# Performance work log

Hardware: AMD Instinct MI355X
Metric: run time of the kernel (lower is better)

The kernel has to match this reference:

```python
import jax, jax.numpy as jnp
import numpy as np

VOCAB = 30
D_MODEL = 512
D_K = 64
D_V = 64
N_HEAD = 8
D_FF = 2048
N_LAYERS = 4
LN_EPS = 1e-5


def _make_pe(max_len, d_model):
    pos = np.arange(max_len, dtype=np.float32)[:, None]
    div = np.exp(np.arange(0, d_model, 2, dtype=np.float32) * (-np.log(10000.0) / d_model))
    pe = np.zeros((max_len, d_model), dtype=np.float32)
    pe[:, 0::2] = np.sin(pos * div)
    pe[:, 1::2] = np.cos(pos * div)
    return jnp.asarray(pe)


def setup_inputs() -> dict:
    key = jax.random.key(0)
    ks = jax.random.split(key, 16)
    B, S = 4, 2048
    s = 0.02
    inp = {
        "input_ids": jax.random.randint(ks[0], (B, S), 0, VOCAB, dtype=jnp.int64),
        "attn_mask": jax.random.randint(ks[1], (B, S), 0, 2, dtype=jnp.int64),
        "tok_embed": jax.random.normal(ks[2], (VOCAB, D_MODEL), jnp.float32) * s,
        "pe": _make_pe(S, D_MODEL),
        "Wq": jax.random.normal(ks[3], (N_LAYERS, D_MODEL, N_HEAD * D_K), jnp.float32) * s,
        "Wk": jax.random.normal(ks[4], (N_LAYERS, D_MODEL, N_HEAD * D_K), jnp.float32) * s,
        "Wv": jax.random.normal(ks[5], (N_LAYERS, D_MODEL, N_HEAD * D_V), jnp.float32) * s,
        "Wo": jax.random.normal(ks[6], (N_LAYERS, N_HEAD * D_V, D_MODEL), jnp.float32) * s,
        "ln1_g": jnp.ones((N_LAYERS, D_MODEL), jnp.float32),
        "ln1_b": jnp.zeros((N_LAYERS, D_MODEL), jnp.float32),
        "W1": jax.random.normal(ks[7], (N_LAYERS, D_MODEL, D_FF), jnp.float32) * s,
        "W2": jax.random.normal(ks[8], (N_LAYERS, D_FF, D_MODEL), jnp.float32) * s,
        "ln2_g": jnp.ones((N_LAYERS, D_MODEL), jnp.float32),
        "ln2_b": jnp.zeros((N_LAYERS, D_MODEL), jnp.float32),
    }
    return inp


def _layernorm(x, g, b):
    mu = jnp.mean(x, axis=-1, keepdims=True)
    var = jnp.mean(jnp.square(x - mu), axis=-1, keepdims=True)
    return (x - mu) * jax.lax.rsqrt(var + LN_EPS) * g + b


def reference(input_ids, attn_mask, tok_embed, pe, Wq, Wk, Wv, Wo, ln1_g, ln1_b, W1, W2, ln2_g, ln2_b):
    B, S = input_ids.shape
    x = tok_embed[input_ids] + pe[:S][None]  # [B,S,D]
    # pad mask: key positions where attn_mask==0, broadcast over heads & queries
    pad = (attn_mask == 0)[:, None, None, :]  # [B,1,1,S]
    scale = 1.0 / np.sqrt(D_K)
    for l in range(N_LAYERS):
        # multi-head self-attention
        q = (x @ Wq[l]).reshape(B, S, N_HEAD, D_K)
        k = (x @ Wk[l]).reshape(B, S, N_HEAD, D_K)
        v = (x @ Wv[l]).reshape(B, S, N_HEAD, D_V)
        scores = jnp.einsum('bqhd,bkhd->bhqk', q, k) * scale
        scores = jnp.where(pad, -1e9, scores)
        attn = jax.nn.softmax(scores, axis=-1)
        ctx = jnp.einsum('bhqk,bkhd->bqhd', attn, v).reshape(B, S, N_HEAD * D_V)
        x = _layernorm(ctx @ Wo[l] + x, ln1_g[l], ln1_b[l])
        # position-wise FFN
        h = jax.nn.relu(x @ W1[l])
        x = _layernorm(h @ W2[l] + x, ln2_g[l], ln2_b[l])
    return x
```

## Files before the change

### kernel.cpp

```cpp
#include <hip/hip_runtime.h>
#include <stdint.h>

#define S_LEN 2048
#define B_SZ 4
#define DM 512
#define NTOK (B_SZ * S_LEN)

typedef unsigned short u16;
typedef unsigned int u32;
typedef unsigned long long u64;
typedef __attribute__((ext_vector_type(8))) short short8;
typedef __attribute__((ext_vector_type(4))) float f32x4;

typedef const __attribute__((address_space(1))) u32 gq_t;
typedef __attribute__((address_space(3))) u32 lq_t;

__device__ __forceinline__ u16 f2bf(float f) {
  union { float f; u32 u; } v; v.f = f;
  return (u16)((v.u + 0x7FFFu + ((v.u >> 16) & 1u)) >> 16);
}

__device__ __forceinline__ float bf2f(u32 hi16_at_lo) {
  union { u32 u; float f; } v; v.u = hi16_at_lo;
  return v.f;
}

__device__ __forceinline__ float fexp2(float x) {
#if __has_builtin(__builtin_amdgcn_exp2f)
  return __builtin_amdgcn_exp2f(x);
#else
  return exp2f(x);
#endif
}

__device__ __forceinline__ short8 mk8(u64 a, u64 b) {
  union { u64 q[2]; short8 s; } u;
  u.q[0] = a; u.q[1] = b;
  return u.s;
}

__device__ __forceinline__ void swap32(u32& x, u32& y) {
  asm("v_permlane32_swap_b32 %0, %1" : "+v"(x), "+v"(y));
}
__device__ __forceinline__ void swap16(u32& x, u32& y, int lane) {
#if __has_builtin(__builtin_amdgcn_permlane16_swap)
  asm("v_permlane16_swap_b32 %0, %1" : "+v"(x), "+v"(y));
#else
  u32 tx = __builtin_amdgcn_ds_swizzle(x, 0x401F);
  u32 ty = __builtin_amdgcn_ds_swizzle(y, 0x401F);
  bool up = (lane & 16) != 0;
  u32 nx = up ? ty : x;
  u32 ny = up ? y : tx;
  x = nx; y = ny;
#endif
}

__global__ void embed_kernel(const int* __restrict__ ids, const float* __restrict__ te,
                             const float* __restrict__ pe, u16* __restrict__ xb) {
  int gid = blockIdx.x * 256 + threadIdx.x;
  int tok = gid >> 7, c4 = (gid & 127) << 2;
  int s = tok & (S_LEN - 1);
  int id = ids[tok];
  const float4 a = *(const float4*)(te + (long)id * DM + c4);
  const float4 p = *(const float4*)(pe + (long)s * DM + c4);
  uint2 pk;
  pk.x = (u32)f2bf(a.x + p.x) | ((u32)f2bf(a.y + p.y) << 16);
  pk.y = (u32)f2bf(a.z + p.z) | ((u32)f2bf(a.w + p.w) << 16);
  *(uint2*)(xb + (long)tok * DM + c4) = pk;
}

__global__ void wconv_all(const float* __restrict__ Wq, const float* __restrict__ Wk,
                          const float* __restrict__ Wv, const float* __restrict__ Wo,
                          const float* __restrict__ W1, const float* __restrict__ W2,
                          u16* __restrict__ WqkvT, u16* __restrict__ WoT,
                          u16* __restrict__ W1T, u16* __restrict__ W2T) {
  __shared__ u16 t_lds[64 * 65];
  const int tile = blockIdx.x;
  const float* src; u16* dst; int N, K, kt, nt, l;
  if (tile < 768) {
    int which = tile >> 8, r = tile & 255;
    l = r >> 6; int rr = r & 63; kt = rr >> 3; nt = rr & 7;
    src = (which == 0 ? Wq : which == 1 ? Wk : Wv) + (long)l * 512 * 512;
    N = 512; K = 512;
    dst = WqkvT + (long)l * 1536 * 512 + (long)(which * 512) * 512;
  } else if (tile < 1024) {
    int r = tile - 768;
    l = r >> 6; int rr = r & 63; kt = rr >> 3; nt = rr & 7;
    src = Wo + (long)l * 512 * 512; N = 512; K = 512;
    dst = WoT + (long)l * 512 * 512;
  } else if (tile < 2048) {
    int r = tile - 1024;
    l = r >> 8; int rr = r & 255; kt = rr >> 5; nt = rr & 31;
    src = W1 + (long)l * 512 * 2048; N = 2048; K = 512;
    dst = W1T + (long)l * 2048 * 512;
  } else {
    int r = tile - 2048;
    l = r >> 8; int rr = r & 255; kt = rr >> 3; nt = rr & 7;
    src = W2 + (long)l * 2048 * 512; N = 512; K = 2048;
    dst = W2T + (long)l * 512 * 2048;
  }
  const int tr = threadIdx.x >> 4;
  const int tc = (threadIdx.x & 15) << 2;
#pragma unroll
  for (int i = 0; i < 4; ++i) {
    int k = tr + i * 16;
    const float4 v = *(const float4*)(src + (long)(kt * 64 + k) * N + nt * 64 + tc);
    t_lds[(tc + 0) * 65 + k] = f2bf(v.x);
    t_lds[(tc + 1) * 65 + k] = f2bf(v.y);
    t_lds[(tc + 2) * 65 + k] = f2bf(v.z);
    t_lds[(tc + 3) * 65 + k] = f2bf(v.w);
  }
  __syncthreads();
#pragma unroll
  for (int i = 0; i < 4; ++i) {
    int n = tr + i * 16;
    u16 a0 = t_lds[n * 65 + tc + 0];
    u16 a1 = t_lds[n * 65 + tc + 1];
    u16 a2 = t_lds[n * 65 + tc + 2];
    u16 a3 = t_lds[n * 65 + tc + 3];
    uint2 pk;
    pk.x = (u32)a0 | ((u32)a1 << 16);
    pk.y = (u32)a2 | ((u32)a3 << 16);
    *(uint2*)(dst + (long)(nt * 64 + n) * K + kt * 64 + tc) = pk;
  }
}

template <int BM, int BN, bool RELU, bool VSPLIT, bool SWAPC>
__global__ __launch_bounds__(BM * 2) void gemm_kernel(const u16* __restrict__ A,
                                                      const u16* __restrict__ BT,
                                                      void* __restrict__ Cout,
                                                      u16* __restrict__ vt,
                                                      int M, int N, int K) {
  constexpr int NI = BN / 32;
  constexpr int NW = BM / 32;
  constexpr int BRW = BN / NW;
  constexpr int LOADS = 4 + BRW / 8;
  __shared__ __align__(16) u16 a_t[2][BM * 64];
  __shared__ __align__(16) u16 b_t[2][BN * 64];
  const int tid = threadIdx.x;
  const int w = tid >> 6, lane = tid & 63;
  const int wr = w >> 1, wc = w & 1;
  const int g = lane >> 4, lr = lane & 15;
  const int l8 = lane >> 3, lch = lane & 7;
  const int gc = lch ^ l8;
  const int nwg = gridDim.x * gridDim.y;
  const int bid = blockIdx.x + gridDim.x * blockIdx.y;
  const int cpx = nwg >> 3;
  const int swz = (bid & 7) * cpx + (bid >> 3);
  const int bx = swz % gridDim.x, by = swz / gridDim.x;
  const long m0 = (long)by * BM, n0 = (long)bx * BN;
  f32x4 acc[4][NI] = {};
  const int nk = K >> 6;

  auto stage = [&](int nb, int kt) {
    const int k0 = kt << 6;
#pragma unroll
    for (int i = 0; i < 4; ++i) {
      int row = w * 32 + i * 8 + l8;
      __builtin_amdgcn_global_load_lds((gq_t*)(A + (m0 + row) * K + k0 + gc * 8),
                                       (lq_t*)&a_t[nb][(w * 4 + i) * 512], 16, 0, 0);
    }
#pragma unroll
    for (int i = 0; i < BRW / 8; ++i) {
      int row = w * BRW + i * 8 + l8;
      __builtin_amdgcn_global_load_lds((gq_t*)(BT + (n0 + row) * K + k0 + gc * 8),
                                       (lq_t*)&b_t[nb][(w * (BRW / 8) + i) * 512], 16, 0, 0);
    }
  };

  stage(0, 0);
  stage(1, 1);
  for (int kt = 0; kt < nk; ++kt) {
    const int cur = kt & 1;
    if (kt + 1 < nk) {
      if constexpr (LOADS == 6) asm volatile("s_waitcnt vmcnt(6)" ::: "memory");
      else                      asm volatile("s_waitcnt vmcnt(5)" ::: "memory");
    } else {
      asm volatile("s_waitcnt vmcnt(0)" ::: "memory");
    }
    __builtin_amdgcn_s_barrier();
    __builtin_amdgcn_sched_barrier(0);
    short8 af[2][4], bfr[2][NI];
#pragma unroll
    for (int ks = 0; ks < 2; ++ks) {
#pragma unroll
      for (int mi = 0; mi < 4; ++mi) {
        int row = wr * 64 + mi * 16 + lr;
        int byte = row * 128 + (((ks * 4 + g) ^ (row & 7)) << 4);
        af[ks][mi] = *(const short8*)((const char*)a_t[cur] + byte);
      }
#pragma unroll
      for (int ni = 0; ni < NI; ++ni) {
        int row = wc * (BN / 2) + ni * 16 + lr;
        int byte = row * 128 + (((ks * 4 + g) ^ (row & 7)) << 4);
        bfr[ks][ni] = *(const short8*)((const char*)b_t[cur] + byte);
      }
    }
    asm volatile("s_waitcnt lgkmcnt(0)" ::: "memory");
    __builtin_amdgcn_s_barrier();
    __builtin_amdgcn_sched_barrier(0);
    if (kt + 2 < nk) stage(cur, kt + 2);
    __builtin_amdgcn_s_setprio(1);
#pragma unroll
    for (int ks = 0; ks < 2; ++ks)
#pragma unroll
      for (int mi = 0; mi < 4; ++mi)
#pragma unroll
        for (int ni = 0; ni < NI; ++ni) {
          if constexpr (SWAPC)
            acc[mi][ni] = __builtin_amdgcn_mfma_f32_16x16x32_bf16(bfr[ks][ni], af[ks][mi], acc[mi][ni], 0, 0, 0);
          else
            acc[mi][ni] = __builtin_amdgcn_mfma_f32_16x16x32_bf16(af[ks][mi], bfr[ks][ni], acc[mi][ni], 0, 0, 0);
        }
    __builtin_amdgcn_s_setprio(0);
  }

  if constexpr (VSPLIT) {
    if (n0 >= 1024) {
#pragma unroll
      for (int mi = 0; mi < 4; ++mi)
#pragma unroll
        for (int ni = 0; ni < NI; ++ni) {
          int vc = (int)(n0 - 1024) + wc * (BN / 2) + ni * 16 + lr;
          int hh = vc >> 6, d = vc & 63;
          long tok0 = m0 + wr * 64 + mi * 16 + g * 4;
          int bb = (int)(tok0 >> 11), s0 = (int)(tok0 & 2047);
          uint2 pk;
          pk.x = (u32)f2bf(acc[mi][ni][0]) | ((u32)f2bf(acc[mi][ni][1]) << 16);
          pk.y = (u32)f2bf(acc[mi][ni][2]) | ((u32)f2bf(acc[mi][ni][3]) << 16);
          *(uint2*)(vt + (((long)bb * 8 + hh) * 64 + d) * 2048 + s0) = pk;
        }
      return;
    }
  }
  if constexpr (SWAPC) {
#pragma unroll
    for (int mi = 0; mi < 4; ++mi)
#pragma unroll
      for (int ni = 0; ni < NI; ++ni) {
        long grow = m0 + wr * 64 + mi * 16 + lr;
        long gcb = n0 + wc * (BN / 2) + ni * 16 + 4 * g;
        float v0 = acc[mi][ni][0], v1 = acc[mi][ni][1], v2 = acc[mi][ni][2], v3 = acc[mi][ni][3];
        if (RELU) {
          v0 = fmaxf(v0, 0.f); v1 = fmaxf(v1, 0.f); v2 = fmaxf(v2, 0.f); v3 = fmaxf(v3, 0.f);
        }
        uint2 pk;
        pk.x = (u32)f2bf(v0) | ((u32)f2bf(v1) << 16);
        pk.y = (u32)f2bf(v2) | ((u32)f2bf(v3) << 16);
        *(uint2*)((u16*)Cout + grow * N + gcb) = pk;
      }
  } else {
#pragma unroll
    for (int mi = 0; mi < 4; ++mi)
#pragma unroll
      for (int ni = 0; ni < NI; ++ni)
#pragma unroll
        for (int j = 0; j < 4; ++j) {
          long grow = m0 + wr * 64 + mi * 16 + g * 4 + j;
          long gcol = n0 + wc * (BN / 2) + ni * 16 + lr;
          float v = acc[mi][ni][j];
          if (RELU) v = fmaxf(v, 0.f);
          ((u16*)Cout)[grow * N + gcol] = f2bf(v);
        }
  }
}

__global__ __launch_bounds__(512) void attn_kernel(const u16* __restrict__ qkv,
                                                   const u16* __restrict__ vt,
                                                   const int* __restrict__ mask,
                                                   u16* __restrict__ ctx) {
  __shared__ __align__(16) u16 kv[2 * 4096 + 2 * 4096 + 1024];
  __shared__ __align__(16) float mvals[2][64];
  __shared__ __align__(16) float l_lds[128];
  const int tid = threadIdx.x;
  const int w = tid >> 6, lane = tid & 63;
  const int g = lane >> 4, lr = lane & 15;
  const int l8 = lane >> 3, lch = lane & 7;
  const int gc = lch ^ l8;
  const int b = blockIdx.z, h = blockIdx.y, q0 = blockIdx.x * 128;
  const long base = (long)b * S_LEN * 1536;
  const int qcol = h * 64, kcol = 512 + h * 64;
  const u16* vhead = vt + (((long)b * 8 + h) * 64) * 2048;
  u16* q_t = kv;
  u16* vone = kv + 16384;
  const float SC = 0.18033688011112042f;

  auto stageKV = [&](int nb, int kb) {
    int row = w * 8 + l8;
    __builtin_amdgcn_global_load_lds((gq_t*)(qkv + base + (long)(kb + row) * 1536 + kcol + gc * 8),
                                     (lq_t*)(kv + nb * 4096 + w * 512), 16, 0, 0);
    __builtin_amdgcn_global_load_lds((gq_t*)(vhead + (long)row * 2048 + kb + gc * 8),
                                     (lq_t*)(kv + 8192 + nb * 4096 + w * 512), 16, 0, 0);
    if (tid < 64) mvals[nb][tid] = (mask[b * S_LEN + kb + tid] == 0) ? -1e9f : 0.f;
  };

  {
    u32 val = ((tid >> 5) == 0) ? 0x3F803F80u : 0u;
    *(u32*)((char*)vone + tid * 4) = val;
  }
#pragma unroll
  for (int i = 0; i < 2; ++i) {
    int e = i * 512 + tid;
    int row = e >> 3, ch = e & 7;
    uint4 v = *(const uint4*)(qkv + base + (long)(q0 + row) * 1536 + qcol + ch * 8);
    *(uint4*)((char*)q_t + row * 128 + ((ch ^ (row & 7)) << 4)) = v;
  }
  __syncthreads();
  short8 qf[2];
#pragma unroll
  for (int ks = 0; ks < 2; ++ks) {
    int row = w * 16 + lr;
    qf[ks] = *(const short8*)((const char*)q_t + row * 128 + (((ks * 4 + g) ^ (row & 7)) << 4));
  }
  __syncthreads();
  stageKV(0, 0);
  __syncthreads();

  f32x4 o[5] = {};

  for (int kt = 0; kt < S_LEN / 64; ++kt) {
    const int cur = kt & 1;
    if (kt + 1 < S_LEN / 64) stageKV(cur ^ 1, (kt + 1) * 64);

    f32x4 s[4] = {};
    __builtin_amdgcn_s_setprio(1);
#pragma unroll
    for (int ks = 0; ks < 2; ++ks) {
#pragma unroll
      for (int ni = 0; ni < 4; ++ni) {
        int row = ni * 16 + lr;
        short8 kf = *(const short8*)((const char*)(kv + cur * 4096) + row * 128 + (((ks * 4 + g) ^ (row & 7)) << 4));
        s[ni] = __builtin_amdgcn_mfma_f32_16x16x32_bf16(kf, qf[ks], s[ni], 0, 0, 0);
      }
    }
    __builtin_amdgcn_s_setprio(0);
    float p[4][4];
#pragma unroll
    for (int ni = 0; ni < 4; ++ni) {
      const float4 mv = *(const float4*)&mvals[cur][ni * 16 + 4 * g];
      const float mva[4] = {mv.x, mv.y, mv.z, mv.w};
#pragma unroll
      for (int r = 0; r < 4; ++r)
        p[ni][r] = fexp2(fmaf(s[ni][r], SC, mva[r]));
    }
    u32 wv[4][2];
#pragma unroll
    for (int ni = 0; ni < 4; ++ni)
#pragma unroll
      for (int pp = 0; pp < 2; ++pp)
        asm("v_cvt_pk_bf16_f32 %0, %1, %2"
            : "=v"(wv[ni][pp]) : "v"(p[ni][2 * pp]), "v"(p[ni][2 * pp + 1]));

    u32 x0 = wv[0][0], x1 = wv[0][1], y0 = wv[1][0], y1 = wv[1][1];
    swap32(x0, y0); swap32(x1, y1);
    swap16(x0, y0, lane); swap16(x1, y1, lane);
    short8 pa0 = mk8((u64)x0 | ((u64)x1 << 32), (u64)y0 | ((u64)y1 << 32));
    u32 x2 = wv[2][0], x3 = wv[2][1], y2 = wv[3][0], y3 = wv[3][1];
    swap32(x2, y2); swap32(x3, y3);
    swap16(x2, y2, lane); swap16(x3, y3, lane);
    short8 pa1 = mk8((u64)x2 | ((u64)x3 << 32), (u64)y2 | ((u64)y3 << 32));

    __builtin_amdgcn_s_setprio(1);
#pragma unroll
    for (int ks2 = 0; ks2 < 2; ++ks2) {
      short8 pa = ks2 ? pa1 : pa0;
#pragma unroll
      for (int nd = 0; nd < 5; ++nd) {
        short8 vf;
        if (nd < 4) {
          int vrow = nd * 16 + lr;
          vf = *(const short8*)((const char*)(kv + 8192 + cur * 4096) + vrow * 128 + (((ks2 * 4 + g) ^ (vrow & 7)) << 4));
        } else {
          vf = *(const short8*)((const char*)vone + lr * 128 + (((ks2 * 4 + g) ^ (lr & 7)) << 4));
        }
        o[nd] = __builtin_amdgcn_mfma_f32_16x16x32_bf16(pa, vf, o[nd], 0, 0, 0);
      }
    }
    __builtin_amdgcn_s_setprio(0);
    if (kt + 1 < S_LEN / 64) __syncthreads();
  }
  if (lr == 0) {
#pragma unroll
    for (int r = 0; r < 4; ++r) l_lds[w * 16 + 4 * g + r] = o[4][r];
  }
  const float4 lv = *(const float4*)&l_lds[w * 16 + 4 * g];
  const float la[4] = {lv.x, lv.y, lv.z, lv.w};
  float inv[4];
#pragma unroll
  for (int r = 0; r < 4; ++r) inv[r] = 1.f / la[r];
#pragma unroll
  for (int nd = 0; nd < 4; ++nd)
#pragma unroll
    for (int r = 0; r < 4; ++r) {
      int tok = q0 + w * 16 + 4 * g + r;
      int col = h * 64 + nd * 16 + lr;
      ctx[((long)b * S_LEN + tok) * 512 + col] = f2bf(o[nd][r] * inv[r]);
    }
}

template <bool FINAL>
__global__ __launch_bounds__(256) void ln_kernel(const u16* __restrict__ y,
                                                 const u16* __restrict__ res,
                                                 const float* __restrict__ gam,
                                                 const float* __restrict__ bet,
                                                 u16* __restrict__ xout,
                                                 float* __restrict__ outf) {
  const int row = blockIdx.x, t = threadIdx.x;
  const long o0 = (long)row * DM;
  const u32 yb = *(const u32*)(y + o0 + 2 * t);
  const u32 rb = *(const u32*)(res + o0 + 2 * t);
  float a0 = bf2f(yb << 16) + bf2f(rb << 16);
  float a1 = bf2f(yb & 0xFFFF0000u) + bf2f(rb & 0xFFFF0000u);
  float s1 = a0 + a1, s2 = a0 * a0 + a1 * a1;
#pragma unroll
  for (int m = 32; m >= 1; m >>= 1) {
    s1 += __shfl_xor(s1, m);
    s2 += __shfl_xor(s2, m);
  }
  __shared__ float w1[4], w2[4];
  if ((t & 63) == 0) { w1[t >> 6] = s1; w2[t >> 6] = s2; }
  __syncthreads();
  s1 = w1[0] + w1[1] + w1[2] + w1[3];
  s2 = w2[0] + w2[1] + w2[2] + w2[3];
  const float mu = s1 * (1.f / DM);
  const float rstd = rsqrtf(s2 * (1.f / DM) - mu * mu + 1e-5f);
  const float2 gv = *(const float2*)&gam[2 * t];
  const float2 bv = *(const float2*)&bet[2 * t];
  float r0 = (a0 - mu) * rstd * gv.x + bv.x;
  float r1 = (a1 - mu) * rstd * gv.y + bv.y;
  if constexpr (FINAL) {
    float2 ov; ov.x = r0; ov.y = r1;
    *(float2*)&outf[o0 + 2 * t] = ov;
  } else {
    u32 pk = (u32)f2bf(r0) | ((u32)f2bf(r1) << 16);
    *(u32*)&xout[o0 + 2 * t] = pk;
  }
}

extern "C" void kernel_launch(void* const* d_in, const int* in_sizes, int n_in,
                              void* d_out, int out_size, void* d_ws, size_t ws_size,
                              hipStream_t stream) {
  const int*   ids  = (const int*)d_in[0];
  const int*   amsk = (const int*)d_in[1];
  const float* te   = (const float*)d_in[2];
  const float* pe   = (const float*)d_in[3];
  const float* Wq   = (const float*)d_in[4];
  const float* Wk   = (const float*)d_in[5];
  const float* Wv   = (const float*)d_in[6];
  const float* Wo   = (const float*)d_in[7];
  const float* ln1g = (const float*)d_in[8];
  const float* ln1b = (const float*)d_in[9];
  const float* W1   = (const float*)d_in[10];
  const float* W2   = (const float*)d_in[11];
  const float* ln2g = (const float*)d_in[12];
  const float* ln2b = (const float*)d_in[13];
  float* out = (float*)d_out;

  char* p = (char*)d_ws;
  u16* x     = (u16*)p;   p += (long)NTOK * DM * 2;
  u16* qkv   = (u16*)p;   p += (long)NTOK * 1536 * 2;
  u16* ctx   = (u16*)p;   p += (long)NTOK * DM * 2;
  u16* tmp   = (u16*)p;   p += (long)NTOK * DM * 2;
  u16* hb    = (u16*)p;   p += (long)NTOK * 2048 * 2;
  u16* WqkvT = (u16*)p;   p += (long)4 * 1536 * 512 * 2;
  u16* WoT   = (u16*)p;   p += (long)4 * 512 * 512 * 2;
  u16* W1T   = (u16*)p;   p += (long)4 * 2048 * 512 * 2;
  u16* W2T   = (u16*)p;   p += (long)4 * 512 * 2048 * 2;
  if ((size_t)(p - (char*)d_ws) > ws_size) return;
  u16* vt = hb;

  wconv_all<<<3072, 256, 0, stream>>>(Wq, Wk, Wv, Wo, W1, W2, WqkvT, WoT, W1T, W2T);
  embed_kernel<<<NTOK * 128 / 256, 256, 0, stream>>>(ids, te, pe, x);

  for (int l = 0; l < 4; ++l) {
    gemm_kernel<256, 64, false, true, false><<<dim3(1536 / 64, NTOK / 256), 512, 0, stream>>>(
        x, WqkvT + (long)l * 1536 * 512, qkv, vt, NTOK, 1536, 512);
    attn_kernel<<<dim3(S_LEN / 128, 8, B_SZ), 512, 0, stream>>>(qkv, vt, amsk, ctx);
    gemm_kernel<128, 64, false, false, true><<<dim3(512 / 64, NTOK / 128), 256, 0, stream>>>(
        ctx, WoT + (long)l * 512 * 512, tmp, nullptr, NTOK, 512, 512);
    ln_kernel<false><<<NTOK, 256, 0, stream>>>(tmp, x, ln1g + l * 512, ln1b + l * 512, x, nullptr);
    gemm_kernel<256, 64, true, false, true><<<dim3(2048 / 64, NTOK / 256), 512, 0, stream>>>(
        x, W1T + (long)l * 2048 * 512, hb, nullptr, NTOK, 2048, 512);
    gemm_kernel<128, 64, false, false, true><<<dim3(512 / 64, NTOK / 128), 256, 0, stream>>>(
        hb, W2T + (long)l * 512 * 2048, tmp, nullptr, NTOK, 512, 2048);
    if (l == 3)
      ln_kernel<true><<<NTOK, 256, 0, stream>>>(tmp, x, ln2g + l * 512, ln2b + l * 512, nullptr, out);
    else
      ln_kernel<false><<<NTOK, 256, 0, stream>>>(tmp, x, ln2g + l * 512, ln2b + l * 512, x, nullptr);
  }
}
```

Measured before the change: 593.4 us.

## Compact valid key positions so attention skips padded keys

Adds a per-batch compaction kernel that builds a list of unmasked key indices, a reverse map and a valid count. The QKV GEMM epilogue scatters V into compacted positions. The attention kernel gathers K rows through the index list and loops only over ceil(nvalid/64) key tiles, masking only the tail. Padded keys contribute exactly zero after softmax, so this drops their share of attention work. In exchange, V stores in the GEMM epilogue become scattered 2-byte writes instead of packed 8-byte writes, and an all-masked row would divide by zero.

```diff
diff --git a/kernel.cpp b/kernel.cpp
--- a/kernel.cpp
+++ b/kernel.cpp
@@ -53,6 +53,37 @@
   u32 ny = up ? y : tx;
   x = nx; y = ny;
 #endif
+}
+
+__global__ void compact_kernel(const int* __restrict__ mask, int* __restrict__ cidx,
+                               int* __restrict__ cmap, int* __restrict__ nvalid) {
+  __shared__ int wcnt[4];
+  __shared__ int running;
+  const int b = blockIdx.x, tid = threadIdx.x;
+  if (tid == 0) running = 0;
+  __syncthreads();
+  for (int c = 0; c < 8; ++c) {
+    int s = c * 256 + tid;
+    int valid = (mask[b * 2048 + s] != 0) ? 1 : 0;
+    u64 bal = __ballot(valid);
+    int lane = tid & 63, wv = tid >> 6;
+    int pre = __popcll(bal & ((1ULL << lane) - 1ULL));
+    if (lane == 0) wcnt[wv] = __popcll(bal);
+    __syncthreads();
+    int woff = running;
+    for (int j = 0; j < wv; ++j) woff += wcnt[j];
+    int pos = woff + pre;
+    if (valid) {
+      cidx[b * 2048 + pos] = s;
+      cmap[b * 2048 + s] = pos;
+    } else {
+      cmap[b * 2048 + s] = -1;
+    }
+    __syncthreads();
+    if (tid == 0) running += wcnt[0] + wcnt[1] + wcnt[2] + wcnt[3];
+    __syncthreads();
+  }
+  if (tid == 0) nvalid[b] = running;
 }
 
 __global__ void embed_kernel(const int* __restrict__ ids, const float* __restrict__ te,
@@ -130,6 +161,7 @@
                                                       const u16* __restrict__ BT,
                                                       void* __restrict__ Cout,
                                                       u16* __restrict__ vt,
+                                                      const int* __restrict__ cmap,
                                                       int M, int N, int K) {
   constexpr int NI = BN / 32;
   constexpr int NW = BM / 32;
@@ -218,18 +250,21 @@
   if constexpr (VSPLIT) {
     if (n0 >= 1024) {
 #pragma unroll
-      for (int mi = 0; mi < 4; ++mi)
-#pragma unroll
-        for (int ni = 0; ni < NI; ++ni) {
-          int vc = (int)(n0 - 1024) + wc * (BN / 2) + ni * 16 + lr;
-          int hh = vc >> 6, d = vc & 63;
-          long tok0 = m0 + wr * 64 + mi * 16 + g * 4;
-          int bb = (int)(tok0 >> 11), s0 = (int)(tok0 & 2047);
-          uint2 pk;
-          pk.x = (u32)f2bf(acc[mi][ni][0]) | ((u32)f2bf(acc[mi][ni][1]) << 16);
-          pk.y = (u32)f2bf(acc[mi][ni][2]) | ((u32)f2bf(acc[mi][ni][3]) << 16);
-          *(uint2*)(vt + (((long)bb * 8 + hh) * 64 + d) * 2048 + s0) = pk;
+      for (int mi = 0; mi < 4; ++mi) {
+        long tok0 = m0 + wr * 64 + mi * 16 + g * 4;
+#pragma unroll
+        for (int j = 0; j < 4; ++j) {
+          int cs = cmap[tok0 + j];
+          if (cs < 0) continue;
+          int bb = (int)((tok0 + j) >> 11);
+#pragma unroll
+          for (int ni = 0; ni < NI; ++ni) {
+            int vc = (int)(n0 - 1024) + wc * (BN / 2) + ni * 16 + lr;
+            int hh = vc >> 6, d = vc & 63;
+            vt[(((long)bb * 8 + hh) * 64 + d) * 2048 + cs] = f2bf(acc[mi][ni][j]);
+          }
         }
+      }
       return;
     }
   }
@@ -267,7 +302,8 @@
 
 __global__ __launch_bounds__(512) void attn_kernel(const u16* __restrict__ qkv,
                                                    const u16* __restrict__ vt,
-                                                   const int* __restrict__ mask,
+                                                   const int* __restrict__ cidx,
+                                                   const int* __restrict__ nvalid,
                                                    u16* __restrict__ ctx) {
   __shared__ __align__(16) u16 kv[2 * 4096 + 2 * 4096 + 1024];
   __shared__ __align__(16) float mvals[2][64];
@@ -284,14 +320,18 @@
   u16* q_t = kv;
   u16* vone = kv + 16384;
   const float SC = 0.18033688011112042f;
+  const int nv = nvalid[b];
+  const int nt = (nv + 63) >> 6;
 
   auto stageKV = [&](int nb, int kb) {
+    int kr = kb + w * 8 + l8;
+    int cs = (kr < nv) ? cidx[b * 2048 + kr] : 0;
+    __builtin_amdgcn_global_load_lds((gq_t*)(qkv + base + (long)cs * 1536 + kcol + gc * 8),
+                                     (lq_t*)(kv + nb * 4096 + w * 512), 16, 0, 0);
     int row = w * 8 + l8;
-    __builtin_amdgcn_global_load_lds((gq_t*)(qkv + base + (long)(kb + row) * 1536 + kcol + gc * 8),
-                                     (lq_t*)(kv + nb * 4096 + w * 512), 16, 0, 0);
     __builtin_amdgcn_global_load_lds((gq_t*)(vhead + (long)row * 2048 + kb + gc * 8),
                                      (lq_t*)(kv + 8192 + nb * 4096 + w * 512), 16, 0, 0);
-    if (tid < 64) mvals[nb][tid] = (mask[b * S_LEN + kb + tid] == 0) ? -1e9f : 0.f;
+    if (tid < 64) mvals[nb][tid] = (kb + tid < nv) ? 0.f : -1e9f;
   };
 
   {
@@ -318,9 +358,9 @@
 
   f32x4 o[5] = {};
 
-  for (int kt = 0; kt < S_LEN / 64; ++kt) {
+  for (int kt = 0; kt < nt; ++kt) {
     const int cur = kt & 1;
-    if (kt + 1 < S_LEN / 64) stageKV(cur ^ 1, (kt + 1) * 64);
+    if (kt + 1 < nt) stageKV(cur ^ 1, (kt + 1) * 64);
 
     f32x4 s[4] = {};
     __builtin_amdgcn_s_setprio(1);
@@ -377,7 +417,7 @@
       }
     }
     __builtin_amdgcn_s_setprio(0);
-    if (kt + 1 < S_LEN / 64) __syncthreads();
+    if (kt + 1 < nt) __syncthreads();
   }
   if (lr == 0) {
 #pragma unroll
@@ -466,23 +506,27 @@
   u16* WoT   = (u16*)p;   p += (long)4 * 512 * 512 * 2;
   u16* W1T   = (u16*)p;   p += (long)4 * 2048 * 512 * 2;
   u16* W2T   = (u16*)p;   p += (long)4 * 512 * 2048 * 2;
+  int* cidx  = (int*)p;   p += (long)B_SZ * S_LEN * 4;
+  int* cmap  = (int*)p;   p += (long)B_SZ * S_LEN * 4;
+  int* nval  = (int*)p;   p += 64;
   if ((size_t)(p - (char*)d_ws) > ws_size) return;
   u16* vt = hb;
 
+  compact_kernel<<<B_SZ, 256, 0, stream>>>(amsk, cidx, cmap, nval);
   wconv_all<<<3072, 256, 0, stream>>>(Wq, Wk, Wv, Wo, W1, W2, WqkvT, WoT, W1T, W2T);
   embed_kernel<<<NTOK * 128 / 256, 256, 0, stream>>>(ids, te, pe, x);
 
   for (int l = 0; l < 4; ++l) {
     gemm_kernel<256, 64, false, true, false><<<dim3(1536 / 64, NTOK / 256), 512, 0, stream>>>(
-        x, WqkvT + (long)l * 1536 * 512, qkv, vt, NTOK, 1536, 512);
-    attn_kernel<<<dim3(S_LEN / 128, 8, B_SZ), 512, 0, stream>>>(qkv, vt, amsk, ctx);
+        x, WqkvT + (long)l * 1536 * 512, qkv, vt, cmap, NTOK, 1536, 512);
+    attn_kernel<<<dim3(S_LEN / 128, 8, B_SZ), 512, 0, stream>>>(qkv, vt, cidx, nval, ctx);
     gemm_kernel<128, 64, false, false, true><<<dim3(512 / 64, NTOK / 128), 256, 0, stream>>>(
-        ctx, WoT + (long)l * 512 * 512, tmp, nullptr, NTOK, 512, 512);
+        ctx, WoT + (long)l * 512 * 512, tmp, nullptr, nullptr, NTOK, 512, 512);
     ln_kernel<false><<<NTOK, 256, 0, stream>>>(tmp, x, ln1g + l * 512, ln1b + l * 512, x, nullptr);
     gemm_kernel<256, 64, true, false, true><<<dim3(2048 / 64, NTOK / 256), 512, 0, stream>>>(
-        x, W1T + (long)l * 2048 * 512, hb, nullptr, NTOK, 2048, 512);
+        x, W1T + (long)l * 2048 * 512, hb, nullptr, nullptr, NTOK, 2048, 512);
     gemm_kernel<128, 64, false, false, true><<<dim3(512 / 64, NTOK / 128), 256, 0, stream>>>(
-        hb, W2T + (long)l * 512 * 2048, tmp, nullptr, NTOK, 512, 2048);
+        hb, W2T + (long)l * 512 * 2048, tmp, nullptr, nullptr, NTOK, 512, 2048);
     if (l == 3)
       ln_kernel<true><<<NTOK, 256, 0, stream>>>(tmp, x, ln2g + l * 512, ln2b + l * 512, nullptr, out);
     else
```

Result: faster. 559.8 us, median of 2 (-5.7%).
